# Performance work log

Hardware: AMD Instinct MI355X
Metric: run time of the kernel (lower is better)

Reference implementation:

```python
import jax, jax.numpy as jnp
import numpy as np

B, C, H, W = 8, 256, 64, 64
N = 3  # num_param
EPS = 1e-5


def conv2d(x, w, b=None, stride=(1, 1), padding=((0, 0), (0, 0)), dilation=(1, 1), groups=1):
    out = jax.lax.conv_general_dilated(
        x, w, window_strides=stride, padding=padding, rhs_dilation=dilation,
        dimension_numbers=('NCHW', 'OIHW', 'NCHW'), feature_group_count=groups)
    if b is not None:
        out = out + b[None, :, None, None]
    return out


def akconv(x, p_w, p_b, ak_w, ak_gamma, ak_beta):
    b, c, h, w = x.shape
    offset = conv2d(x, p_w, p_b, padding=((1, 1), (1, 1)))  # (b, 2N, h, w)
    # initial kernel offsets p_n for num_param=3: rows [0,0,1], cols [0,1,0]
    p_n = jnp.concatenate([jnp.array([0., 0., 1.]), jnp.array([0., 1., 0.])]).reshape(1, 2 * N, 1, 1)
    gx = jnp.broadcast_to(jnp.arange(h, dtype=x.dtype)[:, None], (h, w))
    gy = jnp.broadcast_to(jnp.arange(w, dtype=x.dtype)[None, :], (h, w))
    p_0 = jnp.concatenate([jnp.tile(gx[None, None], (1, N, 1, 1)),
                           jnp.tile(gy[None, None], (1, N, 1, 1))], axis=1)  # (1, 2N, h, w)
    p = p_0 + p_n + offset                      # (b, 2N, h, w)
    p = jnp.transpose(p, (0, 2, 3, 1))          # (b, h, w, 2N)
    q = jnp.floor(jax.lax.stop_gradient(p))
    q_lt_x = jnp.clip(q[..., :N], 0, h - 1)
    q_lt_y = jnp.clip(q[..., N:], 0, w - 1)
    q_rb_x = jnp.clip(q[..., :N] + 1, 0, h - 1)
    q_rb_y = jnp.clip(q[..., N:] + 1, 0, w - 1)
    px = jnp.clip(p[..., :N], 0, h - 1)
    py = jnp.clip(p[..., N:], 0, w - 1)
    # bilinear weights (b, h, w, N)
    g_lt = (1 + (q_lt_x - px)) * (1 + (q_lt_y - py))
    g_rb = (1 - (q_rb_x - px)) * (1 - (q_rb_y - py))
    g_lb = (1 + (q_lt_x - px)) * (1 - (q_rb_y - py))
    g_rt = (1 - (q_rb_x - px)) * (1 + (q_lt_y - py))

    x_flat = x.reshape(b, c, h * w)

    def gather(qx, qy):
        idx = (qx * w + qy).astype(jnp.int32).reshape(b, -1)  # (b, h*w*N)
        out = jnp.take_along_axis(x_flat, idx[:, None, :], axis=2)
        return out.reshape(b, c, h, w, N)

    x_off = (g_lt[:, None] * gather(q_lt_x, q_lt_y)
             + g_rb[:, None] * gather(q_rb_x, q_rb_y)
             + g_lb[:, None] * gather(q_lt_x, q_rb_y)
             + g_rt[:, None] * gather(q_rb_x, q_lt_y))   # (b, c, h, w, N)
    # rearrange 'b c h w n -> b c (h n) w'
    x_off = jnp.transpose(x_off, (0, 1, 2, 4, 3)).reshape(b, c, h * N, w)
    out = conv2d(x_off, ak_w, None, stride=(N, 1))        # (b, c, h, w)
    # BatchNorm2d in training mode (batch statistics) + SiLU
    mean = out.mean(axis=(0, 2, 3), keepdims=True)
    var = ((out - mean) ** 2).mean(axis=(0, 2, 3), keepdims=True)
    out = (out - mean) / jnp.sqrt(var + EPS) * ak_gamma[None, :, None, None] + ak_beta[None, :, None, None]
    return jax.nn.silu(out)


def lka(x, w0, b0, ws, bs, w1, b1):
    u = x
    attn = conv2d(x, w0, b0, padding=((2, 2), (2, 2)), groups=C)                       # 5x5 depthwise
    attn = conv2d(attn, ws, bs, padding=((9, 9), (9, 9)), dilation=(3, 3), groups=C)   # 7x7 dw, dil 3
    attn = conv2d(attn, w1, b1)                                                        # 1x1
    return u * attn


def setup_inputs() -> dict:
    key = jax.random.key(0)
    ks = jax.random.split(key, 8)
    return {
        'x': jax.random.normal(ks[0], (B, C, H, W), jnp.float32),
        'p_w': jax.random.normal(ks[1], (2 * N, C, 3, 3), jnp.float32) * 0.01,
        'p_b': jnp.zeros((2 * N,), jnp.float32),
        'ak_w': jax.random.normal(ks[2], (C, C, 3, 1), jnp.float32) * 0.05,
        'ak_gamma': jnp.ones((C,), jnp.float32),
        'ak_beta': jnp.zeros((C,), jnp.float32),
        'lka0_w': jax.random.normal(ks[3], (C, 1, 5, 5), jnp.float32) * 0.05,
        'lka0_b': jnp.zeros((C,), jnp.float32),
        'lkas_w': jax.random.normal(ks[4], (C, 1, 7, 7), jnp.float32) * 0.05,
        'lkas_b': jnp.zeros((C,), jnp.float32),
        'lka1_w': jax.random.normal(ks[5], (C, C, 1, 1), jnp.float32) * 0.05,
        'lka1_b': jnp.zeros((C,), jnp.float32),
        'conv_w': jax.random.normal(ks[6], (C, C, 1, 1), jnp.float32) * 0.05,
        'conv_b': jnp.zeros((C,), jnp.float32),
    }


def reference(x, p_w, p_b, ak_w, ak_gamma, ak_beta, lka0_w, lka0_b, lkas_w, lkas_b, lka1_w, lka1_b, conv_w, conv_b):
    res = x
    y = akconv(x, p_w, p_b, ak_w, ak_gamma, ak_beta)
    y = lka(y, lka0_w, lka0_b, lkas_w, lkas_b, lka1_w, lka1_b)
    y = conv2d(y, conv_w, conv_b)
    return y + res
```

## Files before the change

### kernel.cpp

```cpp
#include <hip/hip_runtime.h>
#include <math.h>
#include <stdint.h>

#define B_ 8
#define C_ 256
#define HW_ 4096
#define NPIX 32768
#define NELEM (B_*C_*HW_)

typedef __attribute__((ext_vector_type(8))) short short8;
typedef __attribute__((ext_vector_type(4))) float f32x4;

__device__ __forceinline__ unsigned short f2bf(float f) {
    union { float f; uint32_t u; } v; v.f = f;
    uint32_t r = v.u + 0x7FFFu + ((v.u >> 16) & 1u);
    return (unsigned short)(r >> 16);
}
__device__ __forceinline__ float b2f(unsigned short h) {
    union { uint32_t u; float f; } v; v.u = ((uint32_t)h) << 16; return v.f;
}
__device__ __forceinline__ float silu_f(float v) { return v / (1.f + __expf(-v)); }

__device__ __forceinline__ float4 up4(uint2 v) {
    float4 r;
    r.x = b2f((unsigned short)(v.x & 0xffffu));
    r.y = b2f((unsigned short)(v.x >> 16));
    r.z = b2f((unsigned short)(v.y & 0xffffu));
    r.w = b2f((unsigned short)(v.y >> 16));
    return r;
}

__device__ __forceinline__ void gl2lds16(const void* g, void* l) {
    __builtin_amdgcn_global_load_lds(
        (const __attribute__((address_space(1))) void*)g,
        (__attribute__((address_space(3))) void*)l,
        16, 0, 0);
}

__global__ __launch_bounds__(256) void prep_kernel(
    const float* __restrict__ akw, const float* __restrict__ l1w,
    const float* __restrict__ cvw, const float* __restrict__ pw,
    unsigned short* __restrict__ wak, unsigned short* __restrict__ wl1,
    unsigned short* __restrict__ wcv, float* __restrict__ pwt)
{
    int gid = blockIdx.x * 256 + threadIdx.x;
    if (gid < 196608) {
        int e = gid & 7;
        int co = (gid >> 3) & 255;
        int q = gid >> 11;
        int kpp = q * 8 + e;
        int n = kpp >> 8, ci = kpp & 255;
        wak[gid] = f2bf(akw[co * 768 + ci * 3 + n]);
    }
    else if (gid < 262144) {
        int g = gid - 196608;
        int e = g & 7, co = (g >> 3) & 255, q = g >> 11;
        wl1[g] = f2bf(l1w[co * 256 + q * 8 + e]);
    }
    else if (gid < 327680) {
        int g = gid - 262144;
        int e = g & 7, co = (g >> 3) & 255, q = g >> 11;
        wcv[g] = f2bf(cvw[co * 256 + q * 8 + e]);
    }
    else if (gid < 346112) {
        int idx = gid - 327680;
        int ci = idx / 72, r = idx - ci * 72;
        int tt = r / 12, t9 = r - tt * 12;
        pwt[idx] = (t9 < 9) ? pw[tt * 2304 + ci * 9 + t9] : 0.f;
    }
}

__global__ __launch_bounds__(256) void transpose_kernel(
    const float* __restrict__ x, unsigned short* __restrict__ xt)
{
    int blk = blockIdx.x;
    int b = blk & 7;
    int rest = blk >> 3;
    int half = rest & 1, i = rest >> 1;
    int bi = b * 64 + i;
    int tid = threadIdx.x;
    __shared__ float tile[64 * 132];

    {
        int ci_l = tid >> 6, jj = tid & 63;
        const float* ip = x + ((size_t)b * C_ + half * 128 + ci_l) * HW_ + i * 64 + jj;
        #pragma unroll 4
        for (int it = 0; it < 32; ++it)
            tile[jj * 132 + ci_l + it * 4] = ip[(size_t)it * 4 * HW_];
    }
    __syncthreads();
    {
        int j = tid >> 2, q = tid & 3;
        unsigned short* op = xt + ((size_t)(bi * 64 + j)) * 256 + half * 128 + q * 32;
        const float* tp = &tile[j * 132 + q * 32];
        #pragma unroll
        for (int f = 0; f < 4; ++f) {
            union { unsigned short h[8]; uint4 u; } pk;
            #pragma unroll
            for (int e = 0; e < 8; ++e) pk.h[e] = f2bf(tp[f * 8 + e]);
            *(uint4*)(op + f * 8) = pk.u;
        }
    }
}

__global__ __launch_bounds__(256) void offset_s1_kernel(
    const float* __restrict__ x, const float* __restrict__ pwt,
    float* __restrict__ part)
{
    int blk = blockIdx.x;
    int b = blk & 7;
    int rest = blk >> 3;
    int g = rest & 7, i = rest >> 3;
    int bi = b * 64 + i;
    int tid = threadIdx.x;

    __shared__ float tile[6600];

    {
        int cs = tid >> 3, r8 = tid & 7;
        const float* xp = x + ((size_t)b * C_ + g * 32 + cs) * HW_;
        #pragma unroll
        for (int t = 0; t < 6; ++t) {
            int idx = r8 * 6 + t;
            int r = idx >> 4, v4 = idx & 15;
            int ii = i + r - 1;
            float4 val = make_float4(0.f, 0.f, 0.f, 0.f);
            if (ii >= 0 && ii < 64)
                val = *(const float4*)(xp + ii * 64 + v4 * 4);
            int base = (r * 66 + 1 + v4 * 4) * 33 + cs;
            tile[base]      = val.x;  tile[base + 33]  = val.y;
            tile[base + 66] = val.z;  tile[base + 99]  = val.w;
        }
        if (tid < 192) {
            int ci = tid / 6, rem = tid - ci * 6;
            int ki = rem >> 1, side = rem & 1;
            tile[(ki * 66 + side * 65) * 33 + ci] = 0.f;
        }
    }
    __syncthreads();

    int sub = tid >> 4;
    int jq  = tid & 15;

    float acc[6][4];
    #pragma unroll
    for (int tt = 0; tt < 6; ++tt)
        #pragma unroll
        for (int p = 0; p < 4; ++p) acc[tt][p] = 0.f;

    #pragma unroll
    for (int t = 0; t < 2; ++t) {
        int ci = sub + 16 * t;
        float xv[3][6];
        #pragma unroll
        for (int ki = 0; ki < 3; ++ki)
            #pragma unroll
            for (int cc = 0; cc < 6; ++cc)
                xv[ki][cc] = tile[(ki * 66 + jq * 4 + cc) * 33 + ci];
        const float* wp = pwt + (g * 32 + ci) * 72;
        #pragma unroll
        for (int tt = 0; tt < 6; ++tt) {
            float w[9];
            *(float4*)&w[0] = *(const float4*)(wp + tt * 12);
            *(float4*)&w[4] = *(const float4*)(wp + tt * 12 + 4);
            w[8] = wp[tt * 12 + 8];
            #pragma unroll
            for (int ki = 0; ki < 3; ++ki)
                #pragma unroll
                for (int kj = 0; kj < 3; ++kj) {
                    float wgt = w[ki * 3 + kj];
                    #pragma unroll
                    for (int p = 0; p < 4; ++p)
                        acc[tt][p] += wgt * xv[ki][kj + p];
                }
        }
    }

    __syncthreads();
    {
        float* s2 = tile + sub * 387;
        #pragma unroll
        for (int tt = 0; tt < 6; ++tt)
            #pragma unroll
            for (int p = 0; p < 4; ++p)
                s2[tt * 64 + jq * 4 + p] = acc[tt][p];
    }
    __syncthreads();
    size_t pslot = (size_t)bi * 8 + g;
    for (int idx = tid; idx < 384; idx += 256) {
        float s = 0.f;
        #pragma unroll
        for (int sb = 0; sb < 16; ++sb)
            s += tile[sb * 387 + idx];
        part[pslot * 384 + idx] = s;
    }
}

__global__ __launch_bounds__(256) void offset_s2_kernel(
    const float* __restrict__ part, const float* __restrict__ pb,
    int2* __restrict__ tbl_off, float4* __restrict__ tbl_w)
{
    int pix = blockIdx.x * 256 + threadIdx.x;
    int b = pix >> 12, rem = pix & 4095, i = rem >> 6, j = rem & 63;
    int bi = b * 64 + i;
    float v[6];
    #pragma unroll
    for (int tt = 0; tt < 6; ++tt) v[tt] = pb[tt];
    for (int g = 0; g < 8; ++g) {
        const float* pp = part + ((size_t)bi * 8 + g) * 384;
        #pragma unroll
        for (int tt = 0; tt < 6; ++tt) v[tt] += pp[tt * 64 + j];
    }
    const float pnx[3] = {0.f, 0.f, 1.f};
    const float pny[3] = {0.f, 1.f, 0.f};
    #pragma unroll
    for (int n = 0; n < 3; ++n) {
        float px_ = (float)i + pnx[n] + v[n];
        float py_ = (float)j + pny[n] + v[n + 3];
        float qx = floorf(px_), qy = floorf(py_);
        float qlx = fminf(fmaxf(qx,       0.f), 63.f);
        float qly = fminf(fmaxf(qy,       0.f), 63.f);
        float qrx = fminf(fmaxf(qx + 1.f, 0.f), 63.f);
        float qry = fminf(fmaxf(qy + 1.f, 0.f), 63.f);
        float pxc = fminf(fmaxf(px_,      0.f), 63.f);
        float pyc = fminf(fmaxf(py_,      0.f), 63.f);
        float glt = (1.f + (qlx - pxc)) * (1.f + (qly - pyc));
        float grb = (1.f - (qrx - pxc)) * (1.f - (qry - pyc));
        float glb = (1.f + (qlx - pxc)) * (1.f - (qry - pyc));
        float grt = (1.f - (qrx - pxc)) * (1.f + (qly - pyc));
        int ilx = (int)qlx, irx = (int)qrx;
        int ily = (int)qly, iry = (int)qry;
        int c0; float a0, a1, b0, b1;
        if (ily == iry) {
            if (ily == 0) { c0 = 0;  a0 = glt + glb; a1 = 0.f; b0 = grt + grb; b1 = 0.f; }
            else          { c0 = 62; a0 = 0.f; a1 = glt + glb; b0 = 0.f; b1 = grt + grb; }
        } else { c0 = ily; a0 = glt; a1 = glb; b0 = grt; b1 = grb; }
        int oi = (b * 3 + n) * HW_ + i * 64 + j;
        tbl_off[oi] = make_int2(ilx * 64 + c0, irx * 64 + c0);
        tbl_w[oi]   = make_float4(a0, a1, b0, b1);
    }
}

__global__ __launch_bounds__(256) void gather_kernel(
    const unsigned short* __restrict__ xt, const int2* __restrict__ tbl_off,
    const float4* __restrict__ tbl_w, unsigned short* __restrict__ v)
{
    int blk = blockIdx.x;
    int b = blk & 7;
    int rest = blk >> 3;
    int n = rest >> 6, i = rest & 63;
    int bi = b * 64 + i;
    int tid = threadIdx.x;
    int lane = tid & 63, wv = tid >> 6;
    int ci4 = lane * 4;
    const unsigned short* xb = xt + (size_t)b * 1048576;

    __shared__ unsigned short stile[16640];
    int tCloc = ci4 >> 5;
    int kq = (ci4 >> 3) & 3;
    int e  = ci4 & 7;
    unsigned short* sl = &stile[tCloc * 2080 + kq * 520 + e];

    for (int it0 = 0; it0 < 16; it0 += 4) {
        uint2 A8[4], B8[4], C8[4], D8[4];
        float4 w4[4];
        #pragma unroll
        for (int u = 0; u < 4; ++u) {
            int j = wv * 16 + it0 + u;
            int oi = (b * 3 + n) * HW_ + i * 64 + j;
            int2 off = tbl_off[oi];
            w4[u] = tbl_w[oi];
            const unsigned short* p0 = xb + (size_t)off.x * 256 + ci4;
            const unsigned short* p1 = xb + (size_t)off.y * 256 + ci4;
            A8[u] = *(const uint2*)p0;
            B8[u] = *(const uint2*)(p0 + 256);
            C8[u] = *(const uint2*)p1;
            D8[u] = *(const uint2*)(p1 + 256);
        }
        #pragma unroll
        for (int u = 0; u < 4; ++u) {
            int j = wv * 16 + it0 + u;
            float4 A = up4(A8[u]), Bv = up4(B8[u]), Cv = up4(C8[u]), Dv = up4(D8[u]);
            union { unsigned short h[4]; uint2 q; } pk;
            pk.h[0] = f2bf(w4[u].x*A.x + w4[u].y*Bv.x + w4[u].z*Cv.x + w4[u].w*Dv.x);
            pk.h[1] = f2bf(w4[u].x*A.y + w4[u].y*Bv.y + w4[u].z*Cv.y + w4[u].w*Dv.y);
            pk.h[2] = f2bf(w4[u].x*A.z + w4[u].y*Bv.z + w4[u].z*Cv.z + w4[u].w*Dv.z);
            pk.h[3] = f2bf(w4[u].x*A.w + w4[u].y*Bv.w + w4[u].z*Cv.w + w4[u].w*Dv.w);
            *(uint2*)&sl[j * 8] = pk.q;
        }
    }
    __syncthreads();
    unsigned short* vb = v + ((size_t)bi * 24 + n * 8) * 2048;
    int kqW = tid >> 6, jW = tid & 63;
    #pragma unroll
    for (int tc = 0; tc < 8; ++tc) {
        *(uint4*)&vb[tc * 2048 + kqW * 512 + jW * 8] =
            *(const uint4*)&stile[tc * 2080 + kqW * 520 + jW * 8];
    }
}

__global__ __launch_bounds__(256) void ak_mfma_kernel(
    const unsigned short* __restrict__ v, const unsigned short* __restrict__ W,
    unsigned short* __restrict__ yh, float* __restrict__ p1, float* __restrict__ p2)
{
    int blk = blockIdx.x;
    int b = blk & 7, i = blk >> 3;
    int P = b * 64 + i;
    int tid = threadIdx.x;
    int wv = tid >> 6, lane = tid & 63;
    int quad = lane >> 4, l15 = lane & 15;
    __shared__ __align__(16) unsigned short sA[8192];
    __shared__ __align__(16) unsigned short sB[2048];

    const unsigned short* vP = v + (size_t)P * 24 * 2048;

    f32x4 acc[4][4];
    #pragma unroll
    for (int mt = 0; mt < 4; ++mt)
        #pragma unroll
        for (int nt = 0; nt < 4; ++nt) acc[mt][nt] = (f32x4){0.f, 0.f, 0.f, 0.f};

    for (int t = 0; t < 24; ++t) {
        #pragma unroll
        for (int s = 0; s < 4; ++s)
            gl2lds16(W + ((size_t)(t * 4 + s) * 256 + tid) * 8, &sA[(s * 256 + tid) * 8]);
        gl2lds16(vP + (size_t)t * 2048 + tid * 8, &sB[tid * 8]);
        __syncthreads();
        short8 af[4], bf[4];
        #pragma unroll
        for (int mt = 0; mt < 4; ++mt)
            af[mt] = *(const short8*)&sA[(quad * 256 + wv * 64 + mt * 16 + l15) * 8];
        #pragma unroll
        for (int nt = 0; nt < 4; ++nt)
            bf[nt] = *(const short8*)&sB[(quad * 64 + nt * 16 + l15) * 8];
        #pragma unroll
        for (int mt = 0; mt < 4; ++mt)
            #pragma unroll
            for (int nt = 0; nt < 4; ++nt)
                acc[mt][nt] = __builtin_amdgcn_mfma_f32_16x16x32_bf16(
                    af[mt], bf[nt], acc[mt][nt], 0, 0, 0);
        __syncthreads();
    }
    #pragma unroll
    for (int mt = 0; mt < 4; ++mt) {
        #pragma unroll
        for (int r = 0; r < 4; ++r) {
            int co = wv * 64 + mt * 16 + quad * 4 + r;
            size_t base = ((size_t)b * C_ + co) * HW_ + i * 64;
            float s1 = 0.f, s2 = 0.f;
            #pragma unroll
            for (int nt = 0; nt < 4; ++nt) {
                float val = acc[mt][nt][r];
                s1 += val; s2 += val * val;
                yh[base + nt * 16 + l15] = f2bf(val);
            }
            #pragma unroll
            for (int m = 1; m < 16; m <<= 1) {
                s1 += __shfl_xor(s1, m); s2 += __shfl_xor(s2, m);
            }
            if (l15 == 0) { p1[co * 512 + blk] = s1; p2[co * 512 + blk] = s2; }
        }
    }
}

__global__ __launch_bounds__(256) void bn_stats_kernel(
    const float* __restrict__ p1, const float* __restrict__ p2,
    const float* __restrict__ gamma, const float* __restrict__ beta,
    float* __restrict__ ss)
{
    int co = blockIdx.x, tid = threadIdx.x;
    float a = p1[co * 512 + tid] + p1[co * 512 + 256 + tid];
    float q = p2[co * 512 + tid] + p2[co * 512 + 256 + tid];
    __shared__ float r1[256], r2[256];
    r1[tid] = a; r2[tid] = q; __syncthreads();
    for (int st = 128; st > 0; st >>= 1) {
        if (tid < st) { r1[tid] += r1[tid + st]; r2[tid] += r2[tid + st]; }
        __syncthreads();
    }
    if (tid == 0) {
        const float inv_n = 1.f / (float)NPIX;
        float m = r1[0] * inv_n;
        float var = r2[0] * inv_n - m * m;
        float sc = gamma[co] * rsqrtf(var + 1e-5f);
        ss[co] = sc; ss[256 + co] = beta[co] - m * sc;
    }
}

__global__ __launch_bounds__(256) void dw5_fused_kernel(
    const unsigned short* __restrict__ in, const float* __restrict__ ss,
    const float* __restrict__ w, const float* __restrict__ bias,
    unsigned short* __restrict__ out)
{
    int blkI = blockIdx.x;
    int b = blkI & 7, c = blkI >> 3;
    int bc = b * 256 + c;
    int tid = threadIdx.x;
    __shared__ float tile[68 * 68];
    float sc = ss[c], sh = ss[256 + c];
    const unsigned short* ip = in + (size_t)bc * HW_;
    for (int s = tid; s < 68 * 68; s += 256) {
        int r = s / 68, cc = s - r * 68;
        int ii = r - 2, jj = cc - 2;
        float vv = 0.f;
        if (ii >= 0 && ii < 64 && jj >= 0 && jj < 64) {
            float t = b2f(ip[ii * 64 + jj]) * sc + sh;
            vv = silu_f(t);
        }
        tile[s] = vv;
    }
    float wr[25];
    #pragma unroll
    for (int t = 0; t < 25; ++t) wr[t] = w[c * 25 + t];
    float bv = bias[c];
    __syncthreads();

    int jb = tid & 3, row = tid >> 2;
    int j0 = jb * 16;
    float acc[16];
    #pragma unroll
    for (int j = 0; j < 16; ++j) acc[j] = bv;
    #pragma unroll
    for (int di = 0; di < 5; ++di) {
        const float* tp = &tile[(row + di) * 68 + j0];
        float vv[20];
        #pragma unroll
        for (int q = 0; q < 5; ++q)
            *(float4*)&vv[q * 4] = *(const float4*)(tp + q * 4);
        #pragma unroll
        for (int dj = 0; dj < 5; ++dj) {
            float wv = wr[di * 5 + dj];
            #pragma unroll
            for (int j = 0; j < 16; ++j)
                acc[j] += wv * vv[dj + j];
        }
    }
    unsigned short* op = out + (size_t)bc * HW_ + row * 64 + j0;
    union { unsigned short h[8]; uint4 u; } pk;
    #pragma unroll
    for (int half = 0; half < 2; ++half) {
        #pragma unroll
        for (int j = 0; j < 8; ++j) pk.h[j] = f2bf(acc[half * 8 + j]);
        *(uint4*)&op[half * 8] = pk.u;
    }
}

__global__ __launch_bounds__(256) void dw7d3_kernel(
    const unsigned short* __restrict__ in, const float* __restrict__ w,
    const float* __restrict__ bias, unsigned short* __restrict__ out)
{
    int blkI = blockIdx.x;
    int b = blkI & 7, c = blkI >> 3;
    int bc = b * 256 + c;
    int tid = threadIdx.x;
    __shared__ float tile[82 * 84];
    const unsigned short* ip = in + (size_t)bc * HW_;
    for (int s = tid; s < 82 * 84; s += 256) {
        int r = s / 84, cc = s - r * 84;
        int ii = r - 9, jj = cc - 9;
        float vv = 0.f;
        if (ii >= 0 && ii < 64 && jj >= 0 && jj < 64) vv = b2f(ip[ii * 64 + jj]);
        tile[s] = vv;
    }
    float wr[49];
    #pragma unroll
    for (int t = 0; t < 49; ++t) wr[t] = w[c * 49 + t];
    float bv = bias[c];
    __syncthreads();

    int jb = tid & 3, row = tid >> 2;
    int j0 = jb * 16;
    float acc[16];
    #pragma unroll
    for (int j = 0; j < 16; ++j) acc[j] = bv;
    #pragma unroll
    for (int di = 0; di < 7; ++di) {
        const float* tp = &tile[(row + 3 * di) * 84 + j0];
        float vv[36];
        #pragma unroll
        for (int q = 0; q < 9; ++q)
            *(float4*)&vv[q * 4] = *(const float4*)(tp + q * 4);
        #pragma unroll
        for (int dj = 0; dj < 7; ++dj) {
            float wv = wr[di * 7 + dj];
            #pragma unroll
            for (int j = 0; j < 16; ++j)
                acc[j] += wv * vv[3 * dj + j];
        }
    }
    unsigned short* op = out + (size_t)bc * HW_ + row * 64 + j0;
    union { unsigned short h[8]; uint4 u; } pk;
    #pragma unroll
    for (int half = 0; half < 2; ++half) {
        #pragma unroll
        for (int j = 0; j < 8; ++j) pk.h[j] = f2bf(acc[half * 8 + j]);
        *(uint4*)&op[half * 8] = pk.u;
    }
}

template<int MODE>
__global__ __launch_bounds__(256) void gemm1x1_mfma(
    const unsigned short* __restrict__ in, const unsigned short* __restrict__ W,
    const float* __restrict__ bias,
    const unsigned short* __restrict__ auxh, const float* __restrict__ auxf,
    const float* __restrict__ ss,
    unsigned short* __restrict__ out_bf, float* __restrict__ out_f)
{
    int blk = blockIdx.x;
    int b = blk & 7, i = blk >> 3;
    int tid = threadIdx.x;
    int wv = tid >> 6, lane = tid & 63;
    int quad = lane >> 4, l15 = lane & 15;
    __shared__ __align__(16) unsigned short sA[8192];
    __shared__ __align__(16) unsigned short sB[2048];
    int pixS = tid & 63, kqS = tid >> 6;

    const unsigned short* bp = in + ((size_t)b * C_) * HW_ + i * 64 + pixS;

    f32x4 acc[4][4];
    #pragma unroll
    for (int mt = 0; mt < 4; ++mt)
        #pragma unroll
        for (int nt = 0; nt < 4; ++nt) acc[mt][nt] = (f32x4){0.f, 0.f, 0.f, 0.f};

    for (int t = 0; t < 8; ++t) {
        #pragma unroll
        for (int s = 0; s < 4; ++s)
            gl2lds16(W + ((size_t)(t * 4 + s) * 256 + tid) * 8, &sA[(s * 256 + tid) * 8]);
        {
            const unsigned short* p = bp + (size_t)(t * 32 + kqS * 8) * HW_;
            union { unsigned short h[8]; uint4 u; } hb;
            #pragma unroll
            for (int jj = 0; jj < 8; ++jj) hb.h[jj] = p[(size_t)jj * HW_];
            *(uint4*)&sB[(kqS * 64 + pixS) * 8] = hb.u;
        }
        __syncthreads();
        short8 af[4], bf[4];
        #pragma unroll
        for (int mt = 0; mt < 4; ++mt)
            af[mt] = *(const short8*)&sA[(quad * 256 + wv * 64 + mt * 16 + l15) * 8];
        #pragma unroll
        for (int nt = 0; nt < 4; ++nt)
            bf[nt] = *(const short8*)&sB[(quad * 64 + nt * 16 + l15) * 8];
        #pragma unroll
        for (int mt = 0; mt < 4; ++mt)
            #pragma unroll
            for (int nt = 0; nt < 4; ++nt)
                acc[mt][nt] = __builtin_amdgcn_mfma_f32_16x16x32_bf16(
                    af[mt], bf[nt], acc[mt][nt], 0, 0, 0);
        __syncthreads();
    }
    #pragma unroll
    for (int mt = 0; mt < 4; ++mt) {
        #pragma unroll
        for (int r = 0; r < 4; ++r) {
            int co = wv * 64 + mt * 16 + quad * 4 + r;
            float bco = bias[co];
            size_t base = ((size_t)b * C_ + co) * HW_ + i * 64;
            if (MODE == 0) {
                float sc = ss[co], sh = ss[256 + co];
                #pragma unroll
                for (int nt = 0; nt < 4; ++nt) {
                    int col = nt * 16 + l15;
                    float o = acc[mt][nt][r] + bco;
                    float u = silu_f(b2f(auxh[base + col]) * sc + sh);
                    out_bf[base + col] = f2bf(o * u);
                }
            } else {
                #pragma unroll
                for (int nt = 0; nt < 4; ++nt) {
                    int col = nt * 16 + l15;
                    out_f[base + col] = acc[mt][nt][r] + bco + auxf[base + col];
                }
            }
        }
    }
}

extern "C" void kernel_launch(void* const* d_in, const int* in_sizes, int n_in,
                              void* d_out, int out_size, void* d_ws, size_t ws_size,
                              hipStream_t stream) {
    const float* x     = (const float*)d_in[0];
    const float* p_w   = (const float*)d_in[1];
    const float* p_b   = (const float*)d_in[2];
    const float* ak_w  = (const float*)d_in[3];
    const float* ak_g  = (const float*)d_in[4];
    const float* ak_b  = (const float*)d_in[5];
    const float* l0_w  = (const float*)d_in[6];
    const float* l0_b  = (const float*)d_in[7];
    const float* ls_w  = (const float*)d_in[8];
    const float* ls_b  = (const float*)d_in[9];
    const float* l1_w  = (const float*)d_in[10];
    const float* l1_b  = (const float*)d_in[11];
    const float* cv_w  = (const float*)d_in[12];
    const float* cv_b  = (const float*)d_in[13];
    float* out = (float*)d_out;

    char* w = (char*)d_ws;
    int2*   tbl_off = (int2*)w;
    float4* tbl_w   = (float4*)(w + 786432);
    unsigned short* wak = (unsigned short*)(w + 2359296);
    unsigned short* wl1 = (unsigned short*)(w + 2752512);
    unsigned short* wcv = (unsigned short*)(w + 2883584);
    float* p1 = (float*)(w + 3014656);
    float* p2 = (float*)(w + 3538944);
    float* ss = (float*)(w + 4063232);
    float* pwt = (float*)(w + 4065280);
    unsigned short* xt = (unsigned short*)(w + 4194304);
    unsigned short* ybh    = (unsigned short*)(w + 4194304);
    unsigned short* dw5out = (unsigned short*)(w + 20971520);
    float* part = (float*)(w + 37748736);
    unsigned short* attn   = (unsigned short*)(w + 37748736);
    unsigned short* v      = (unsigned short*)(w + 44040192);
    unsigned short* g0out  = (unsigned short*)(w + 54525952);

    prep_kernel<<<1352, 256, 0, stream>>>(ak_w, l1_w, cv_w, p_w, wak, wl1, wcv, pwt);
    offset_s1_kernel<<<4096, 256, 0, stream>>>(x, pwt, part);
    offset_s2_kernel<<<128, 256, 0, stream>>>(part, p_b, tbl_off, tbl_w);
    transpose_kernel<<<1024, 256, 0, stream>>>(x, xt);
    gather_kernel<<<1536, 256, 0, stream>>>(xt, tbl_off, tbl_w, v);
    ak_mfma_kernel<<<512, 256, 0, stream>>>(v, wak, ybh, p1, p2);
    bn_stats_kernel<<<256, 256, 0, stream>>>(p1, p2, ak_g, ak_b, ss);
    dw5_fused_kernel<<<2048, 256, 0, stream>>>(ybh, ss, l0_w, l0_b, dw5out);
    dw7d3_kernel<<<2048, 256, 0, stream>>>(dw5out, ls_w, ls_b, attn);
    gemm1x1_mfma<0><<<512, 256, 0, stream>>>(attn, wl1, l1_b, ybh, nullptr, ss, g0out, nullptr);
    gemm1x1_mfma<1><<<512, 256, 0, stream>>>(g0out, wcv, cv_b, nullptr, x, nullptr, nullptr, out);
}
```

Before: 278.1 us.

## Fuse depthwise conv pair and 1x1 GEMM pair through LDS intermediates

Merges the 5x5 and dilated 7x7 depthwise convolutions into one kernel that keeps the intermediate in shared memory in fp32. It also merges the gated 1x1 GEMM with the final 1x1 GEMM, staging the gated activation in LDS as the B operand. This removes two global intermediate round trips and two launches. The cost is larger LDS footprints, which lower occupancy, and a slight change in numerics.

```diff
diff --git a/kernel.cpp b/kernel.cpp
--- a/kernel.cpp
+++ b/kernel.cpp
@@ -386,16 +386,21 @@
     }
 }
 
-__global__ __launch_bounds__(256) void dw5_fused_kernel(
+__global__ __launch_bounds__(256) void dw_fused_kernel(
     const unsigned short* __restrict__ in, const float* __restrict__ ss,
-    const float* __restrict__ w, const float* __restrict__ bias,
+    const float* __restrict__ w5, const float* __restrict__ b5,
+    const float* __restrict__ w7, const float* __restrict__ b7,
     unsigned short* __restrict__ out)
 {
     int blkI = blockIdx.x;
     int b = blkI & 7, c = blkI >> 3;
     int bc = b * 256 + c;
     int tid = threadIdx.x;
-    __shared__ float tile[68 * 68];
+    __shared__ float t1[68 * 68];
+    __shared__ float t2[82 * 84];
+
+    for (int s = tid; s < 82 * 84; s += 256) t2[s] = 0.f;
+
     float sc = ss[c], sh = ss[256 + c];
     const unsigned short* ip = in + (size_t)bc * HW_;
     for (int s = tid; s < 68 * 68; s += 256) {
@@ -406,104 +411,80 @@
             float t = b2f(ip[ii * 64 + jj]) * sc + sh;
             vv = silu_f(t);
         }
-        tile[s] = vv;
-    }
-    float wr[25];
-    #pragma unroll
-    for (int t = 0; t < 25; ++t) wr[t] = w[c * 25 + t];
-    float bv = bias[c];
+        t1[s] = vv;
+    }
     __syncthreads();
 
     int jb = tid & 3, row = tid >> 2;
     int j0 = jb * 16;
-    float acc[16];
-    #pragma unroll
-    for (int j = 0; j < 16; ++j) acc[j] = bv;
-    #pragma unroll
-    for (int di = 0; di < 5; ++di) {
-        const float* tp = &tile[(row + di) * 68 + j0];
-        float vv[20];
-        #pragma unroll
-        for (int q = 0; q < 5; ++q)
-            *(float4*)&vv[q * 4] = *(const float4*)(tp + q * 4);
-        #pragma unroll
-        for (int dj = 0; dj < 5; ++dj) {
-            float wv = wr[di * 5 + dj];
-            #pragma unroll
-            for (int j = 0; j < 16; ++j)
-                acc[j] += wv * vv[dj + j];
-        }
-    }
-    unsigned short* op = out + (size_t)bc * HW_ + row * 64 + j0;
-    union { unsigned short h[8]; uint4 u; } pk;
-    #pragma unroll
-    for (int half = 0; half < 2; ++half) {
-        #pragma unroll
-        for (int j = 0; j < 8; ++j) pk.h[j] = f2bf(acc[half * 8 + j]);
-        *(uint4*)&op[half * 8] = pk.u;
-    }
-}
-
-__global__ __launch_bounds__(256) void dw7d3_kernel(
-    const unsigned short* __restrict__ in, const float* __restrict__ w,
-    const float* __restrict__ bias, unsigned short* __restrict__ out)
-{
-    int blkI = blockIdx.x;
-    int b = blkI & 7, c = blkI >> 3;
-    int bc = b * 256 + c;
-    int tid = threadIdx.x;
-    __shared__ float tile[82 * 84];
-    const unsigned short* ip = in + (size_t)bc * HW_;
-    for (int s = tid; s < 82 * 84; s += 256) {
-        int r = s / 84, cc = s - r * 84;
-        int ii = r - 9, jj = cc - 9;
-        float vv = 0.f;
-        if (ii >= 0 && ii < 64 && jj >= 0 && jj < 64) vv = b2f(ip[ii * 64 + jj]);
-        tile[s] = vv;
-    }
-    float wr[49];
-    #pragma unroll
-    for (int t = 0; t < 49; ++t) wr[t] = w[c * 49 + t];
-    float bv = bias[c];
+    {
+        float wr[25];
+        #pragma unroll
+        for (int t = 0; t < 25; ++t) wr[t] = w5[c * 25 + t];
+        float bv = b5[c];
+        float acc[16];
+        #pragma unroll
+        for (int j = 0; j < 16; ++j) acc[j] = bv;
+        #pragma unroll
+        for (int di = 0; di < 5; ++di) {
+            const float* tp = &t1[(row + di) * 68 + j0];
+            float vv[20];
+            #pragma unroll
+            for (int q = 0; q < 5; ++q)
+                *(float4*)&vv[q * 4] = *(const float4*)(tp + q * 4);
+            #pragma unroll
+            for (int dj = 0; dj < 5; ++dj) {
+                float wv = wr[di * 5 + dj];
+                #pragma unroll
+                for (int j = 0; j < 16; ++j)
+                    acc[j] += wv * vv[dj + j];
+            }
+        }
+        float* t2w = &t2[(row + 9) * 84 + 9 + j0];
+        #pragma unroll
+        for (int j = 0; j < 16; ++j) t2w[j] = acc[j];
+    }
     __syncthreads();
-
-    int jb = tid & 3, row = tid >> 2;
-    int j0 = jb * 16;
-    float acc[16];
-    #pragma unroll
-    for (int j = 0; j < 16; ++j) acc[j] = bv;
-    #pragma unroll
-    for (int di = 0; di < 7; ++di) {
-        const float* tp = &tile[(row + 3 * di) * 84 + j0];
-        float vv[36];
-        #pragma unroll
-        for (int q = 0; q < 9; ++q)
-            *(float4*)&vv[q * 4] = *(const float4*)(tp + q * 4);
-        #pragma unroll
-        for (int dj = 0; dj < 7; ++dj) {
-            float wv = wr[di * 7 + dj];
-            #pragma unroll
-            for (int j = 0; j < 16; ++j)
-                acc[j] += wv * vv[3 * dj + j];
-        }
-    }
-    unsigned short* op = out + (size_t)bc * HW_ + row * 64 + j0;
-    union { unsigned short h[8]; uint4 u; } pk;
-    #pragma unroll
-    for (int half = 0; half < 2; ++half) {
-        #pragma unroll
-        for (int j = 0; j < 8; ++j) pk.h[j] = f2bf(acc[half * 8 + j]);
-        *(uint4*)&op[half * 8] = pk.u;
-    }
-}
-
-template<int MODE>
-__global__ __launch_bounds__(256) void gemm1x1_mfma(
-    const unsigned short* __restrict__ in, const unsigned short* __restrict__ W,
-    const float* __restrict__ bias,
-    const unsigned short* __restrict__ auxh, const float* __restrict__ auxf,
-    const float* __restrict__ ss,
-    unsigned short* __restrict__ out_bf, float* __restrict__ out_f)
+    {
+        float wr[49];
+        #pragma unroll
+        for (int t = 0; t < 49; ++t) wr[t] = w7[c * 49 + t];
+        float bv = b7[c];
+        float acc[16];
+        #pragma unroll
+        for (int j = 0; j < 16; ++j) acc[j] = bv;
+        #pragma unroll
+        for (int di = 0; di < 7; ++di) {
+            const float* tp = &t2[(row + 3 * di) * 84 + j0];
+            float vv[36];
+            #pragma unroll
+            for (int q = 0; q < 9; ++q)
+                *(float4*)&vv[q * 4] = *(const float4*)(tp + q * 4);
+            #pragma unroll
+            for (int dj = 0; dj < 7; ++dj) {
+                float wv = wr[di * 7 + dj];
+                #pragma unroll
+                for (int j = 0; j < 16; ++j)
+                    acc[j] += wv * vv[3 * dj + j];
+            }
+        }
+        unsigned short* op = out + (size_t)bc * HW_ + row * 64 + j0;
+        union { unsigned short h[8]; uint4 u; } pk;
+        #pragma unroll
+        for (int half = 0; half < 2; ++half) {
+            #pragma unroll
+            for (int j = 0; j < 8; ++j) pk.h[j] = f2bf(acc[half * 8 + j]);
+            *(uint4*)&op[half * 8] = pk.u;
+        }
+    }
+}
+
+__global__ __launch_bounds__(256) void gemm_fused_kernel(
+    const unsigned short* __restrict__ in,
+    const unsigned short* __restrict__ W0, const float* __restrict__ bias0,
+    const unsigned short* __restrict__ W1, const float* __restrict__ bias1,
+    const unsigned short* __restrict__ auxh, const float* __restrict__ ss,
+    const float* __restrict__ auxf, float* __restrict__ out_f)
 {
     int blk = blockIdx.x;
     int b = blk & 7, i = blk >> 3;
@@ -512,6 +493,7 @@
     int quad = lane >> 4, l15 = lane & 15;
     __shared__ __align__(16) unsigned short sA[8192];
     __shared__ __align__(16) unsigned short sB[2048];
+    __shared__ __align__(16) unsigned short mid[16384];
     int pixS = tid & 63, kqS = tid >> 6;
 
     const unsigned short* bp = in + ((size_t)b * C_) * HW_ + i * 64 + pixS;
@@ -525,7 +507,7 @@
     for (int t = 0; t < 8; ++t) {
         #pragma unroll
         for (int s = 0; s < 4; ++s)
-            gl2lds16(W + ((size_t)(t * 4 + s) * 256 + tid) * 8, &sA[(s * 256 + tid) * 8]);
+            gl2lds16(W0 + ((size_t)(t * 4 + s) * 256 + tid) * 8, &sA[(s * 256 + tid) * 8]);
         {
             const unsigned short* p = bp + (size_t)(t * 32 + kqS * 8) * HW_;
             union { unsigned short h[8]; uint4 u; } hb;
@@ -554,23 +536,53 @@
         #pragma unroll
         for (int r = 0; r < 4; ++r) {
             int co = wv * 64 + mt * 16 + quad * 4 + r;
-            float bco = bias[co];
+            float bco = bias0[co];
             size_t base = ((size_t)b * C_ + co) * HW_ + i * 64;
-            if (MODE == 0) {
-                float sc = ss[co], sh = ss[256 + co];
-                #pragma unroll
-                for (int nt = 0; nt < 4; ++nt) {
-                    int col = nt * 16 + l15;
-                    float o = acc[mt][nt][r] + bco;
-                    float u = silu_f(b2f(auxh[base + col]) * sc + sh);
-                    out_bf[base + col] = f2bf(o * u);
-                }
-            } else {
-                #pragma unroll
-                for (int nt = 0; nt < 4; ++nt) {
-                    int col = nt * 16 + l15;
-                    out_f[base + col] = acc[mt][nt][r] + bco + auxf[base + col];
-                }
+            float sc = ss[co], sh = ss[256 + co];
+            #pragma unroll
+            for (int nt = 0; nt < 4; ++nt) {
+                int col = nt * 16 + l15;
+                float o = acc[mt][nt][r] + bco;
+                float u = silu_f(b2f(auxh[base + col]) * sc + sh);
+                mid[((co >> 3) * 64 + col) * 8 + (co & 7)] = f2bf(o * u);
+            }
+        }
+    }
+    #pragma unroll
+    for (int mt = 0; mt < 4; ++mt)
+        #pragma unroll
+        for (int nt = 0; nt < 4; ++nt) acc[mt][nt] = (f32x4){0.f, 0.f, 0.f, 0.f};
+    for (int t = 0; t < 8; ++t) {
+        #pragma unroll
+        for (int s = 0; s < 4; ++s)
+            gl2lds16(W1 + ((size_t)(t * 4 + s) * 256 + tid) * 8, &sA[(s * 256 + tid) * 8]);
+        __syncthreads();
+        short8 af[4], bf[4];
+        #pragma unroll
+        for (int mt = 0; mt < 4; ++mt)
+            af[mt] = *(const short8*)&sA[(quad * 256 + wv * 64 + mt * 16 + l15) * 8];
+        #pragma unroll
+        for (int nt = 0; nt < 4; ++nt)
+            bf[nt] = *(const short8*)&mid[((t * 4 + quad) * 64 + nt * 16 + l15) * 8];
+        #pragma unroll
+        for (int mt = 0; mt < 4; ++mt)
+            #pragma unroll
+            for (int nt = 0; nt < 4; ++nt)
+                acc[mt][nt] = __builtin_amdgcn_mfma_f32_16x16x32_bf16(
+                    af[mt], bf[nt], acc[mt][nt], 0, 0, 0);
+        __syncthreads();
+    }
+    #pragma unroll
+    for (int mt = 0; mt < 4; ++mt) {
+        #pragma unroll
+        for (int r = 0; r < 4; ++r) {
+            int co = wv * 64 + mt * 16 + quad * 4 + r;
+            float bco = bias1[co];
+            size_t base = ((size_t)b * C_ + co) * HW_ + i * 64;
+            #pragma unroll
+            for (int nt = 0; nt < 4; ++nt) {
+                int col = nt * 16 + l15;
+                out_f[base + col] = acc[mt][nt][r] + bco + auxf[base + col];
             }
         }
     }
@@ -607,11 +619,9 @@
     float* pwt = (float*)(w + 4065280);
     unsigned short* xt = (unsigned short*)(w + 4194304);
     unsigned short* ybh    = (unsigned short*)(w + 4194304);
-    unsigned short* dw5out = (unsigned short*)(w + 20971520);
     float* part = (float*)(w + 37748736);
     unsigned short* attn   = (unsigned short*)(w + 37748736);
     unsigned short* v      = (unsigned short*)(w + 44040192);
-    unsigned short* g0out  = (unsigned short*)(w + 54525952);
 
     prep_kernel<<<1352, 256, 0, stream>>>(ak_w, l1_w, cv_w, p_w, wak, wl1, wcv, pwt);
     offset_s1_kernel<<<4096, 256, 0, stream>>>(x, pwt, part);
@@ -620,8 +630,6 @@
     gather_kernel<<<1536, 256, 0, stream>>>(xt, tbl_off, tbl_w, v);
     ak_mfma_kernel<<<512, 256, 0, stream>>>(v, wak, ybh, p1, p2);
     bn_stats_kernel<<<256, 256, 0, stream>>>(p1, p2, ak_g, ak_b, ss);
-    dw5_fused_kernel<<<2048, 256, 0, stream>>>(ybh, ss, l0_w, l0_b, dw5out);
-    dw7d3_kernel<<<2048, 256, 0, stream>>>(dw5out, ls_w, ls_b, attn);
-    gemm1x1_mfma<0><<<512, 256, 0, stream>>>(attn, wl1, l1_b, ybh, nullptr, ss, g0out, nullptr);
-    gemm1x1_mfma<1><<<512, 256, 0, stream>>>(g0out, wcv, cv_b, nullptr, x, nullptr, nullptr, out);
-}
+    dw_fused_kernel<<<2048, 256, 0, stream>>>(ybh, ss, l0_w, l0_b, ls_w, ls_b, attn);
+    gemm_fused_kernel<<<512, 256, 0, stream>>>(attn, wl1, l1_b, wcv, cv_b, ybh, ss, x, out);
+}
```

New measurement: 271.5 us. -2.4%, faster.
